# Performance work log

Measured on AMD Instinct MI355X. Metric: run time of the kernel, lower is better.

## Reference

```python
import jax, jax.numpy as jnp
import numpy as np

T, H, I, E, K, L, R = 1024, 1024, 1024, 8, 2, 4, 16
N = 2 * I  # gate_up dim


def setup_inputs() -> dict:
    key = jax.random.key(0)
    ks = jax.random.split(key, 12)
    tw = jax.random.uniform(ks[1], (T, K), dtype=jnp.float32) + 0.1
    tw = tw / tw.sum(axis=-1, keepdims=True)  # routing weights sum to 1
    return {
        "hidden_states": jax.random.normal(ks[0], (T, H), dtype=jnp.float32),
        "topk_weights": tw,
        "w13": jax.random.normal(ks[2], (E, N, H), dtype=jnp.float32) * (1.0 / np.sqrt(H)),
        "w2": jax.random.normal(ks[3], (E, H, I), dtype=jnp.float32) * (1.0 / np.sqrt(I)),
        "gate_up_lora_a": jax.random.normal(ks[4], (L, E, R, H), dtype=jnp.float32) * (1.0 / np.sqrt(H)),
        "gate_up_lora_b": jax.random.normal(ks[5], (L, E, N, R), dtype=jnp.float32) * (1.0 / np.sqrt(R)),
        "down_lora_a": jax.random.normal(ks[6], (L, E, R, I), dtype=jnp.float32) * (1.0 / np.sqrt(I)),
        "down_lora_b": jax.random.normal(ks[7], (L, E, H, R), dtype=jnp.float32) * (1.0 / np.sqrt(R)),
        "scalings": jax.random.uniform(ks[8], (L,), dtype=jnp.float32) + 0.5,
        "topk_ids": jax.random.randint(ks[9], (T, K), 0, E, dtype=jnp.int32),
        "lora_indices": jax.random.randint(ks[10], (T,), 0, L, dtype=jnp.int32),
    }


def reference(hidden_states, topk_weights, w13, w2, gate_up_lora_a,
              gate_up_lora_b, down_lora_a, down_lora_b, scalings,
              topk_ids, lora_indices):
    num_tokens, hidden = hidden_states.shape
    num_experts, gate_up_dim, _ = w13.shape
    top_k = topk_ids.shape[1]
    inter = gate_up_dim // 2
    TKp = num_tokens * top_k

    e_flat = topk_ids.reshape(-1)                      # [TK] expert per dispatched pair
    l_flat = jnp.repeat(lora_indices, top_k)           # [TK] adapter per pair
    w_flat = topk_weights.reshape(-1)                  # [TK] routing weight
    x_rep = jnp.repeat(hidden_states, top_k, axis=0)   # [TK, H]

    # ---- grouped gate_up GEMM (base path): cache1[p] = x[p] @ w13[e(p)]^T ----
    cache1 = jnp.zeros((TKp, gate_up_dim), dtype=hidden_states.dtype)
    for ei in range(num_experts):  # small fixed expert count
        mask = (e_flat == ei)[:, None]
        cache1 = cache1 + jnp.where(mask, x_rep @ w13[ei].T, 0.0)

    # ---- per-expert gate_up LoRA delta, injected BEFORE activation ----
    scal = scalings[l_flat][:, None]                   # [TK, 1]
    Ag = gate_up_lora_a[l_flat, e_flat]                # [TK, R, H]
    Bg = gate_up_lora_b[l_flat, e_flat]                # [TK, N, R]
    tmp = jnp.einsum('prh,ph->pr', Ag, x_rep)
    cache1 = cache1 + jnp.einsum('pnr,pr->pn', Bg, tmp) * scal

    # ---- silu_and_mul on (base + lora) ----
    act = jax.nn.silu(cache1[:, :inter]) * cache1[:, inter:]   # [TK, I]

    # ---- grouped down GEMM (base), routed-weight applied ----
    cache3 = jnp.zeros((TKp, hidden), dtype=hidden_states.dtype)
    for ei in range(num_experts):
        mask = (e_flat == ei)[:, None]
        cache3 = cache3 + jnp.where(mask, act @ w2[ei].T, 0.0)
    cache3 = cache3 * w_flat[:, None]

    # ---- per-expert down LoRA delta (weighted by routing weight) ----
    Ad = down_lora_a[l_flat, e_flat]                   # [TK, R, I]
    Bd = down_lora_b[l_flat, e_flat]                   # [TK, H, R]
    tmpd = jnp.einsum('pri,pi->pr', Ad, act)
    cache3 = cache3 + jnp.einsum('phr,pr->ph', Bd, tmpd) * scal * w_flat[:, None]

    # ---- combine expert outputs (moe_sum over top_k slots) ----
    return cache3.reshape(num_tokens, top_k, hidden).sum(axis=1)
```

## Files before the change

kernel.cpp:

```cpp
#include <hip/hip_runtime.h>
#include <stdint.h>

#define Td 1024
#define Hd 1024
#define Id 1024
#define Ed 8
#define Kd 2
#define Ld 4
#define Rd 16
#define Nd 2048
#define TKd (Td*Kd)

typedef __bf16 bf16x8 __attribute__((ext_vector_type(8)));
typedef float f32x4 __attribute__((ext_vector_type(4)));

__device__ __forceinline__ ushort f2bf(float f) {
    uint32_t u = __builtin_bit_cast(uint32_t, f);
    return (ushort)((u + 0x7fffu + ((u >> 16) & 1u)) >> 16);
}
__device__ __forceinline__ float bf2f(ushort u) {
    uint32_t x = ((uint32_t)u) << 16;
    return __builtin_bit_cast(float, x);
}
__device__ __forceinline__ bf16x8 pack8(float4 a, float4 b) {
    bf16x8 r;
    r[0] = (__bf16)a.x; r[1] = (__bf16)a.y; r[2] = (__bf16)a.z; r[3] = (__bf16)a.w;
    r[4] = (__bf16)b.x; r[5] = (__bf16)b.y; r[6] = (__bf16)b.z; r[7] = (__bf16)b.w;
    return r;
}

#define GLOAD_LDS16(g, l) __builtin_amdgcn_global_load_lds( \
    (const __attribute__((address_space(1))) uint32_t*)(const void*)(g), \
    (__attribute__((address_space(3))) uint32_t*)(void*)(l), 16, 0, 0)

#define XB 512
#define CB 384
#define TB 2048
#define ZB 1024
#define PREP_BLOCKS (XB + CB + TB + ZB + 1)

__global__ __launch_bounds__(256) void k_prep(
    const float* __restrict__ hid, const float* __restrict__ gb,
    const float* __restrict__ db, const float* __restrict__ ga,
    const float* __restrict__ sc, const int* __restrict__ tids,
    const int* __restrict__ lidx,
    ushort* __restrict__ xb, ushort* __restrict__ gbbe, ushort* __restrict__ dbbe,
    ushort* __restrict__ tmp1e, float* __restrict__ out,
    int* __restrict__ sorted, int* __restrict__ offs)
{
    __shared__ float tr[Rd];
    __shared__ int cnt[Ed];
    __shared__ int cur[Ed];
    const int b = blockIdx.x, tid = threadIdx.x;

    if (b < XB) {
        int i = b * 256 + tid;
        size_t off = (size_t)i * 8;
        float4 a = *(const float4*)(hid + off);
        float4 c = *(const float4*)(hid + off + 4);
        uint4 o;
        o.x = (uint)f2bf(a.x) | ((uint)f2bf(a.y) << 16);
        o.y = (uint)f2bf(a.z) | ((uint)f2bf(a.w) << 16);
        o.z = (uint)f2bf(c.x) | ((uint)f2bf(c.y) << 16);
        o.w = (uint)f2bf(c.z) | ((uint)f2bf(c.w) << 16);
        *(uint4*)(xb + off) = o;
    } else if (b < XB + CB) {
        constexpr int GR = Ld * Ed * Nd;
        int i = (b - XB) * 256 + tid;
        const float* src; ushort* dst;
        if (i < GR) {
            int l = i >> 14, e = (i >> 11) & 7, n = i & 2047;
            src = gb + (size_t)i * 16;
            dst = gbbe + ((size_t)(e * Nd + n)) * 64 + l * 16;
        } else {
            int j = i - GR;
            int l = j >> 13, e = (j >> 10) & 7, n = j & 1023;
            src = db + (size_t)j * 16;
            dst = dbbe + ((size_t)(e * Id + n)) * 64 + l * 16;
        }
        float4 a0 = *(const float4*)(src);
        float4 a1 = *(const float4*)(src + 4);
        float4 a2 = *(const float4*)(src + 8);
        float4 a3 = *(const float4*)(src + 12);
        uint4 o;
        o.x = (uint)f2bf(a0.x) | ((uint)f2bf(a0.y) << 16);
        o.y = (uint)f2bf(a0.z) | ((uint)f2bf(a0.w) << 16);
        o.z = (uint)f2bf(a1.x) | ((uint)f2bf(a1.y) << 16);
        o.w = (uint)f2bf(a1.z) | ((uint)f2bf(a1.w) << 16);
        *(uint4*)(dst) = o;
        o.x = (uint)f2bf(a2.x) | ((uint)f2bf(a2.y) << 16);
        o.y = (uint)f2bf(a2.z) | ((uint)f2bf(a2.w) << 16);
        o.z = (uint)f2bf(a3.x) | ((uint)f2bf(a3.y) << 16);
        o.w = (uint)f2bf(a3.z) | ((uint)f2bf(a3.w) << 16);
        *(uint4*)(dst + 8) = o;
    } else if (b < XB + CB + TB) {
        const int p = b - XB - CB;
        const int e = tids[p];
        const int l = lidx[p >> 1];
        const float s = sc[l];
        const int r = tid >> 4, q = tid & 15;
        const float* A = ga + (((size_t)l * Ed + e) * Rd + r) * 1024;
        const float* x = hid + (size_t)(p >> 1) * 1024;
        float sum = 0.f;
        #pragma unroll
        for (int i = 0; i < 16; ++i) {
            int h = q * 4 + 64 * i;
            float4 a = *(const float4*)(A + h);
            float4 v = *(const float4*)(x + h);
            sum += a.x * v.x + a.y * v.y + a.z * v.z + a.w * v.w;
        }
        sum += __shfl_xor(sum, 1); sum += __shfl_xor(sum, 2);
        sum += __shfl_xor(sum, 4); sum += __shfl_xor(sum, 8);
        if (q == 0) tr[r] = sum;
        __syncthreads();
        if (tid < 32) {
            int j0 = tid * 2;
            uint v = 0;
            if ((j0 >> 4) == l)
                v = (uint)f2bf(s * tr[j0 & 15]) | ((uint)f2bf(s * tr[(j0 + 1) & 15]) << 16);
            ((uint*)(tmp1e + (size_t)p * 64))[tid] = v;
        }
    } else if (b < XB + CB + TB + ZB) {
        int i = (b - XB - CB - TB) * 256 + tid;
        ((float4*)out)[i] = make_float4(0.f, 0.f, 0.f, 0.f);
    } else {
        if (tid < Ed) cnt[tid] = 0;
        __syncthreads();
        int el[8];
        #pragma unroll
        for (int i = 0; i < 8; ++i) {
            el[i] = tids[tid + i * 256];
            atomicAdd(&cnt[el[i]], 1);
        }
        __syncthreads();
        if (tid == 0) {
            int s = 0;
            for (int e = 0; e < Ed; ++e) { offs[e] = s; cur[e] = s; s += cnt[e]; }
            offs[Ed] = s;
        }
        __syncthreads();
        #pragma unroll
        for (int i = 0; i < 8; ++i) {
            int pos = atomicAdd(&cur[el[i]], 1);
            sorted[pos] = tid + i * 256;
        }
    }
}

__global__ __launch_bounds__(256) void k_tmp_dn(
    const ushort* __restrict__ act, const float* __restrict__ da,
    const float* __restrict__ sc, const int* __restrict__ tids,
    const int* __restrict__ lidx, ushort* __restrict__ tmpde)
{
    const int p = blockIdx.x;
    const int e = tids[p];
    const int l = lidx[p >> 1];
    const float s = sc[l];
    const int tid = threadIdx.x;
    const int r = tid >> 4, q = tid & 15;
    const float* A = da + (((size_t)l * Ed + e) * Rd + r) * 1024;
    const ushort* x = act + (size_t)p * 1024;
    float sum = 0.f;
    #pragma unroll
    for (int i = 0; i < 8; ++i) {
        int h = q * 8 + 128 * i;
        float4 a0 = *(const float4*)(A + h);
        float4 a1 = *(const float4*)(A + h + 4);
        ushort4 v0 = *(const ushort4*)(x + h);
        ushort4 v1 = *(const ushort4*)(x + h + 4);
        sum += a0.x * bf2f(v0.x) + a0.y * bf2f(v0.y) + a0.z * bf2f(v0.z) + a0.w * bf2f(v0.w)
             + a1.x * bf2f(v1.x) + a1.y * bf2f(v1.y) + a1.z * bf2f(v1.z) + a1.w * bf2f(v1.w);
    }
    sum += __shfl_xor(sum, 1); sum += __shfl_xor(sum, 2);
    sum += __shfl_xor(sum, 4); sum += __shfl_xor(sum, 8);
    __shared__ float tr[Rd];
    if (q == 0) tr[r] = sum;
    __syncthreads();
    if (tid < 32) {
        int j0 = tid * 2;
        uint v = 0;
        if ((j0 >> 4) == l)
            v = (uint)f2bf(s * tr[j0 & 15]) | ((uint)f2bf(s * tr[(j0 + 1) & 15]) << 16);
        ((uint*)(tmpde + (size_t)p * 64))[tid] = v;
    }
}

__global__ __launch_bounds__(256) void k_gemm_gu(
    const ushort* __restrict__ xb, const float* __restrict__ w13,
    const ushort* __restrict__ tmp1e, const ushort* __restrict__ gbbe,
    ushort* __restrict__ act, const int* __restrict__ sorted,
    const int* __restrict__ offs)
{
    __shared__ ushort As[2][128][32];
    __shared__ ushort Bs[2][128][32];
    const int tid = threadIdx.x, lane = tid & 63, wave = tid >> 6;
    const int wr = wave >> 1, wc = wave & 1;
    const int fr = lane & 15, fk = (lane >> 4) * 8;

    int off[Ed + 1];
    #pragma unroll
    for (int e = 0; e <= Ed; ++e) off[e] = offs[e];
    int mt[Ed]; int tot = 0;
    #pragma unroll
    for (int e = 0; e < Ed; ++e) {
        mt[e] = (off[e + 1] - off[e] + 127) / 128;
        tot += mt[e] * 16;
    }

    for (int tau = blockIdx.x; tau < tot; tau += gridDim.x) {
        int t = tau, e = 0;
        while (t >= mt[e] * 16) { t -= mt[e] * 16; ++e; }
        const int m0 = off[e] + (t >> 4) * 128;
        const int mend = off[e + 1];
        const int n0 = (t & 15) * 64;

        const ushort *asrc[2], *aesrc[2], *besrc[2];
        #pragma unroll
        for (int r = 0; r < 2; ++r) {
            int c = r * 256 + tid;
            int row = c >> 2, kc = c & 3;
            int aIdx = m0 + row; if (aIdx > mend - 1) aIdx = mend - 1;
            int p = sorted[aIdx];
            asrc[r]  = xb + (size_t)(p >> 1) * 1024 + kc * 8;
            aesrc[r] = tmp1e + (size_t)p * 64 + kc * 8;
            int grow = (row < 64) ? (n0 + row) : (1024 + n0 + row - 64);
            besrc[r] = gbbe + ((size_t)e * Nd + grow) * 64 + kc * 8;
        }
        const int brow = tid >> 1, bhalf = tid & 1;
        const int bg_row = (brow < 64) ? (n0 + brow) : (1024 + n0 + brow - 64);
        const float* bsrc = w13 + ((size_t)e * Nd + bg_row) * 1024 + bhalf * 16;

        f32x4 ag[4][2] = {}, au[4][2] = {};
        auto step = [&](int buf) {
            bf16x8 af[4], bg[2], bu[2];
            #pragma unroll
            for (int mi = 0; mi < 4; ++mi)
                af[mi] = *(const bf16x8*)(&As[buf][wr * 64 + mi * 16 + fr][fk]);
            #pragma unroll
            for (int ni = 0; ni < 2; ++ni) {
                bg[ni] = *(const bf16x8*)(&Bs[buf][wc * 32 + ni * 16 + fr][fk]);
                bu[ni] = *(const bf16x8*)(&Bs[buf][64 + wc * 32 + ni * 16 + fr][fk]);
            }
            #pragma unroll
            for (int mi = 0; mi < 4; ++mi)
                #pragma unroll
                for (int ni = 0; ni < 2; ++ni) {
                    ag[mi][ni] = __builtin_amdgcn_mfma_f32_16x16x32_bf16(af[mi], bg[ni], ag[mi][ni], 0, 0, 0);
                    au[mi][ni] = __builtin_amdgcn_mfma_f32_16x16x32_bf16(af[mi], bu[ni], au[mi][ni], 0, 0, 0);
                }
        };

        #pragma unroll
        for (int r = 0; r < 2; ++r)
            GLOAD_LDS16(asrc[r], (char*)&As[0][0][0] + (r * 256 + wave * 64) * 16);
        {
            float4 y0 = *(const float4*)(bsrc);
            float4 y1 = *(const float4*)(bsrc + 4);
            float4 y2 = *(const float4*)(bsrc + 8);
            float4 y3 = *(const float4*)(bsrc + 12);
            *(bf16x8*)(&Bs[0][brow][bhalf * 16])     = pack8(y0, y1);
            *(bf16x8*)(&Bs[0][brow][bhalf * 16 + 8]) = pack8(y2, y3);
        }
        __syncthreads();

        int buf = 0;
        for (int k0 = 32; k0 < 1024; k0 += 32) {
            #pragma unroll
            for (int r = 0; r < 2; ++r)
                GLOAD_LDS16(asrc[r] + k0, (char*)&As[buf ^ 1][0][0] + (r * 256 + wave * 64) * 16);
            float4 y0 = *(const float4*)(bsrc + k0);
            float4 y1 = *(const float4*)(bsrc + k0 + 4);
            float4 y2 = *(const float4*)(bsrc + k0 + 8);
            float4 y3 = *(const float4*)(bsrc + k0 + 12);

            step(buf);

            *(bf16x8*)(&Bs[buf ^ 1][brow][bhalf * 16])     = pack8(y0, y1);
            *(bf16x8*)(&Bs[buf ^ 1][brow][bhalf * 16 + 8]) = pack8(y2, y3);
            __syncthreads();
            buf ^= 1;
        }
        step(buf);

        #pragma unroll
        for (int es = 0; es < 2; ++es) {
            #pragma unroll
            for (int r = 0; r < 2; ++r) {
                GLOAD_LDS16(aesrc[r] + es * 32, (char*)&As[es][0][0] + (r * 256 + wave * 64) * 16);
                GLOAD_LDS16(besrc[r] + es * 32, (char*)&Bs[es][0][0] + (r * 256 + wave * 64) * 16);
            }
            __syncthreads();
            step(es);
        }

        const int rb = wr * 64 + (lane >> 4) * 4;
        #pragma unroll
        for (int mi = 0; mi < 4; ++mi) {
            #pragma unroll
            for (int j = 0; j < 4; ++j) {
                int sidx = m0 + rb + mi * 16 + j;
                if (sidx < mend) {
                    int p = sorted[sidx];
                    ushort* ar = act + (size_t)p * 1024 + n0 + wc * 32;
                    #pragma unroll
                    for (int ni = 0; ni < 2; ++ni) {
                        float g = ag[mi][ni][j], u = au[mi][ni][j];
                        float v = g / (1.f + __expf(-g)) * u;
                        ar[ni * 16 + fr] = f2bf(v);
                    }
                }
            }
        }
        __syncthreads();
    }
}

__global__ __launch_bounds__(256) void k_gemm_dn(
    const ushort* __restrict__ act, const float* __restrict__ w2,
    const ushort* __restrict__ tmpde, const ushort* __restrict__ dbbe,
    const float* __restrict__ tw, float* __restrict__ out,
    const int* __restrict__ sorted, const int* __restrict__ offs)
{
    __shared__ ushort As[2][128][32];
    __shared__ ushort Bs[2][64][32];
    const int tid = threadIdx.x, lane = tid & 63, wave = tid >> 6;
    const int wr = wave >> 1, wc = wave & 1;
    const int fr = lane & 15, fk = (lane >> 4) * 8;

    int off[Ed + 1];
    #pragma unroll
    for (int e = 0; e <= Ed; ++e) off[e] = offs[e];
    int mt[Ed]; int tot = 0;
    #pragma unroll
    for (int e = 0; e < Ed; ++e) {
        mt[e] = (off[e + 1] - off[e] + 127) / 128;
        tot += mt[e] * 16;
    }

    for (int tau = blockIdx.x; tau < tot; tau += gridDim.x) {
        int t = tau, e = 0;
        while (t >= mt[e] * 16) { t -= mt[e] * 16; ++e; }
        const int m0 = off[e] + (t >> 4) * 128;
        const int mend = off[e + 1];
        const int n0 = (t & 15) * 64;

        const ushort *asrc[2], *aesrc[2], *besrc;
        #pragma unroll
        for (int r = 0; r < 2; ++r) {
            int c = r * 256 + tid;
            int row = c >> 2, kc = c & 3;
            int aIdx = m0 + row; if (aIdx > mend - 1) aIdx = mend - 1;
            int p = sorted[aIdx];
            asrc[r]  = act + (size_t)p * 1024 + kc * 8;
            aesrc[r] = tmpde + (size_t)p * 64 + kc * 8;
        }
        besrc = dbbe + ((size_t)e * Hd + n0 + (tid >> 2)) * 64 + (tid & 3) * 8;
        const int brow = tid >> 2, bq = tid & 3;
        const float* bsrc = w2 + ((size_t)e * Hd + n0 + brow) * 1024 + bq * 8;

        f32x4 acc[4][2] = {};
        auto step = [&](int buf) {
            bf16x8 af[4], bv[2];
            #pragma unroll
            for (int mi = 0; mi < 4; ++mi)
                af[mi] = *(const bf16x8*)(&As[buf][wr * 64 + mi * 16 + fr][fk]);
            #pragma unroll
            for (int ni = 0; ni < 2; ++ni)
                bv[ni] = *(const bf16x8*)(&Bs[buf][wc * 32 + ni * 16 + fr][fk]);
            #pragma unroll
            for (int mi = 0; mi < 4; ++mi)
                #pragma unroll
                for (int ni = 0; ni < 2; ++ni)
                    acc[mi][ni] = __builtin_amdgcn_mfma_f32_16x16x32_bf16(af[mi], bv[ni], acc[mi][ni], 0, 0, 0);
        };

        #pragma unroll
        for (int r = 0; r < 2; ++r)
            GLOAD_LDS16(asrc[r], (char*)&As[0][0][0] + (r * 256 + wave * 64) * 16);
        {
            float4 y0 = *(const float4*)(bsrc);
            float4 y1 = *(const float4*)(bsrc + 4);
            *(bf16x8*)(&Bs[0][brow][bq * 8]) = pack8(y0, y1);
        }
        __syncthreads();

        int buf = 0;
        for (int k0 = 32; k0 < 1024; k0 += 32) {
            #pragma unroll
            for (int r = 0; r < 2; ++r)
                GLOAD_LDS16(asrc[r] + k0, (char*)&As[buf ^ 1][0][0] + (r * 256 + wave * 64) * 16);
            float4 y0 = *(const float4*)(bsrc + k0);
            float4 y1 = *(const float4*)(bsrc + k0 + 4);

            step(buf);

            *(bf16x8*)(&Bs[buf ^ 1][brow][bq * 8]) = pack8(y0, y1);
            __syncthreads();
            buf ^= 1;
        }
        step(buf);

        #pragma unroll
        for (int es = 0; es < 2; ++es) {
            #pragma unroll
            for (int r = 0; r < 2; ++r)
                GLOAD_LDS16(aesrc[r] + es * 32, (char*)&As[es][0][0] + (r * 256 + wave * 64) * 16);
            GLOAD_LDS16(besrc + es * 32, (char*)&Bs[es][0][0] + (wave * 64) * 16);
            __syncthreads();
            step(es);
        }

        const int rb = wr * 64 + (lane >> 4) * 4;
        #pragma unroll
        for (int mi = 0; mi < 4; ++mi) {
            #pragma unroll
            for (int j = 0; j < 4; ++j) {
                int sidx = m0 + rb + mi * 16 + j;
                if (sidx < mend) {
                    int p = sorted[sidx];
                    float w = tw[p];
                    float* orow = out + (size_t)(p >> 1) * 1024 + n0 + wc * 32;
                    #pragma unroll
                    for (int ni = 0; ni < 2; ++ni)
                        atomicAdd(&orow[ni * 16 + fr], w * acc[mi][ni][j]);
                }
            }
        }
        __syncthreads();
    }
}

extern "C" void kernel_launch(void* const* d_in, const int* in_sizes, int n_in,
                              void* d_out, int out_size, void* d_ws, size_t ws_size,
                              hipStream_t stream) {
    const float* hid  = (const float*)d_in[0];
    const float* tw   = (const float*)d_in[1];
    const float* w13  = (const float*)d_in[2];
    const float* w2   = (const float*)d_in[3];
    const float* ga   = (const float*)d_in[4];
    const float* gb   = (const float*)d_in[5];
    const float* da   = (const float*)d_in[6];
    const float* db   = (const float*)d_in[7];
    const float* sc   = (const float*)d_in[8];
    const int*   tids = (const int*)d_in[9];
    const int*   lidx = (const int*)d_in[10];
    float* out = (float*)d_out;

    char* ws = (char*)d_ws;
    ushort* xb     = (ushort*)(ws);
    ushort* gbbe   = (ushort*)(ws + (2ull << 20));
    ushort* dbbe   = (ushort*)(ws + (4ull << 20));
    ushort* tmp1e  = (ushort*)(ws + (5ull << 20));
    ushort* tmpde  = (ushort*)(ws + (5ull << 20) + (256u << 10));
    ushort* act    = (ushort*)(ws + (6ull << 20));
    int*    sorted = (int*)(ws + (10ull << 20));
    int*    offs   = (int*)(ws + (10ull << 20) + TKd * 4);

    k_prep<<<PREP_BLOCKS, 256, 0, stream>>>(hid, gb, db, ga, sc, tids, lidx,
                                            xb, gbbe, dbbe, tmp1e, out, sorted, offs);
    k_gemm_gu<<<512, 256, 0, stream>>>(xb, w13, tmp1e, gbbe, act, sorted, offs);
    k_tmp_dn<<<TKd, 256, 0, stream>>>(act, da, sc, tids, lidx, tmpde);
    k_gemm_dn<<<512, 256, 0, stream>>>(act, w2, tmpde, dbbe, tw, out, sorted, offs);
}
```

Measured before the change: 100.8 us.

## Stream fp32 operands straight to LDS with swizzle, convert to bf16 at fragment load

Result: slower. 156.4 us (+55.2%).

```diff
diff --git a/kernel.cpp b/kernel.cpp
--- a/kernel.cpp
+++ b/kernel.cpp
@@ -33,68 +33,48 @@
     (const __attribute__((address_space(1))) uint32_t*)(const void*)(g), \
     (__attribute__((address_space(3))) uint32_t*)(void*)(l), 16, 0, 0)
 
-#define XB 512
 #define CB 384
 #define TB 2048
 #define ZB 1024
-#define PREP_BLOCKS (XB + CB + TB + ZB + 1)
+#define PREP_BLOCKS (CB + TB + ZB + 1)
 
 __global__ __launch_bounds__(256) void k_prep(
     const float* __restrict__ hid, const float* __restrict__ gb,
     const float* __restrict__ db, const float* __restrict__ ga,
     const float* __restrict__ sc, const int* __restrict__ tids,
     const int* __restrict__ lidx,
-    ushort* __restrict__ xb, ushort* __restrict__ gbbe, ushort* __restrict__ dbbe,
-    ushort* __restrict__ tmp1e, float* __restrict__ out,
-    int* __restrict__ sorted, int* __restrict__ offs)
+    float* __restrict__ gbbe, float* __restrict__ dbbe, float* __restrict__ tmp1e,
+    float* __restrict__ out, int* __restrict__ sorted, int* __restrict__ offs)
 {
     __shared__ float tr[Rd];
     __shared__ int cnt[Ed];
     __shared__ int cur[Ed];
     const int b = blockIdx.x, tid = threadIdx.x;
 
-    if (b < XB) {
+    if (b < CB) {
+        constexpr int GR = Ld * Ed * Nd;
         int i = b * 256 + tid;
-        size_t off = (size_t)i * 8;
-        float4 a = *(const float4*)(hid + off);
-        float4 c = *(const float4*)(hid + off + 4);
-        uint4 o;
-        o.x = (uint)f2bf(a.x) | ((uint)f2bf(a.y) << 16);
-        o.y = (uint)f2bf(a.z) | ((uint)f2bf(a.w) << 16);
-        o.z = (uint)f2bf(c.x) | ((uint)f2bf(c.y) << 16);
-        o.w = (uint)f2bf(c.z) | ((uint)f2bf(c.w) << 16);
-        *(uint4*)(xb + off) = o;
-    } else if (b < XB + CB) {
-        constexpr int GR = Ld * Ed * Nd;
-        int i = (b - XB) * 256 + tid;
-        const float* src; ushort* dst;
+        const float* src; float* dst;
         if (i < GR) {
             int l = i >> 14, e = (i >> 11) & 7, n = i & 2047;
             src = gb + (size_t)i * 16;
             dst = gbbe + ((size_t)(e * Nd + n)) * 64 + l * 16;
         } else {
             int j = i - GR;
-            int l = j >> 13, e = (j >> 10) & 7, n = j & 1023;
+            int l = j >> 13, e = (j >> 10) & 7, h = j & 1023;
             src = db + (size_t)j * 16;
-            dst = dbbe + ((size_t)(e * Id + n)) * 64 + l * 16;
+            dst = dbbe + ((size_t)(e * Id + h)) * 64 + l * 16;
         }
         float4 a0 = *(const float4*)(src);
         float4 a1 = *(const float4*)(src + 4);
         float4 a2 = *(const float4*)(src + 8);
         float4 a3 = *(const float4*)(src + 12);
-        uint4 o;
-        o.x = (uint)f2bf(a0.x) | ((uint)f2bf(a0.y) << 16);
-        o.y = (uint)f2bf(a0.z) | ((uint)f2bf(a0.w) << 16);
-        o.z = (uint)f2bf(a1.x) | ((uint)f2bf(a1.y) << 16);
-        o.w = (uint)f2bf(a1.z) | ((uint)f2bf(a1.w) << 16);
-        *(uint4*)(dst) = o;
-        o.x = (uint)f2bf(a2.x) | ((uint)f2bf(a2.y) << 16);
-        o.y = (uint)f2bf(a2.z) | ((uint)f2bf(a2.w) << 16);
-        o.z = (uint)f2bf(a3.x) | ((uint)f2bf(a3.y) << 16);
-        o.w = (uint)f2bf(a3.z) | ((uint)f2bf(a3.w) << 16);
-        *(uint4*)(dst + 8) = o;
-    } else if (b < XB + CB + TB) {
-        const int p = b - XB - CB;
+        *(float4*)(dst)      = a0;
+        *(float4*)(dst + 4)  = a1;
+        *(float4*)(dst + 8)  = a2;
+        *(float4*)(dst + 12) = a3;
+    } else if (b < CB + TB) {
+        const int p = b - CB;
         const int e = tids[p];
         const int l = lidx[p >> 1];
         const float s = sc[l];
@@ -113,15 +93,11 @@
         sum += __shfl_xor(sum, 4); sum += __shfl_xor(sum, 8);
         if (q == 0) tr[r] = sum;
         __syncthreads();
-        if (tid < 32) {
-            int j0 = tid * 2;
-            uint v = 0;
-            if ((j0 >> 4) == l)
-                v = (uint)f2bf(s * tr[j0 & 15]) | ((uint)f2bf(s * tr[(j0 + 1) & 15]) << 16);
-            ((uint*)(tmp1e + (size_t)p * 64))[tid] = v;
-        }
-    } else if (b < XB + CB + TB + ZB) {
-        int i = (b - XB - CB - TB) * 256 + tid;
+        if (tid < 64) {
+            tmp1e[(size_t)p * 64 + tid] = ((tid >> 4) == l) ? s * tr[tid & 15] : 0.f;
+        }
+    } else if (b < CB + TB + ZB) {
+        int i = (b - CB - TB) * 256 + tid;
         ((float4*)out)[i] = make_float4(0.f, 0.f, 0.f, 0.f);
     } else {
         if (tid < Ed) cnt[tid] = 0;
@@ -186,111 +162,107 @@
 }
 
 __global__ __launch_bounds__(256) void k_gemm_gu(
-    const ushort* __restrict__ xb, const float* __restrict__ w13,
-    const ushort* __restrict__ tmp1e, const ushort* __restrict__ gbbe,
+    const float* __restrict__ hid, const float* __restrict__ w13,
+    const float* __restrict__ tmp1e, const float* __restrict__ gbbe,
     ushort* __restrict__ act, const int* __restrict__ sorted,
     const int* __restrict__ offs)
 {
-    __shared__ ushort As[2][128][32];
-    __shared__ ushort Bs[2][128][32];
+    __shared__ float Af[2][128 * 32];
+    __shared__ float Bf[2][128 * 32];
     const int tid = threadIdx.x, lane = tid & 63, wave = tid >> 6;
     const int wr = wave >> 1, wc = wave & 1;
-    const int fr = lane & 15, fk = (lane >> 4) * 8;
-
-    int off[Ed + 1];
+    const int fr = lane & 15, q = lane >> 4;
+
+    int off[Ed + 1], mt[Ed], pre[Ed + 1];
     #pragma unroll
     for (int e = 0; e <= Ed; ++e) off[e] = offs[e];
-    int mt[Ed]; int tot = 0;
+    pre[0] = 0;
     #pragma unroll
     for (int e = 0; e < Ed; ++e) {
         mt[e] = (off[e + 1] - off[e] + 127) / 128;
-        tot += mt[e] * 16;
-    }
-
-    for (int tau = blockIdx.x; tau < tot; tau += gridDim.x) {
-        int t = tau, e = 0;
-        while (t >= mt[e] * 16) { t -= mt[e] * 16; ++e; }
-        const int m0 = off[e] + (t >> 4) * 128;
+        pre[e + 1] = pre[e] + mt[e] * 16;
+    }
+    const int tot = pre[Ed];
+
+    for (int bid = blockIdx.x; bid < tot; bid += gridDim.x) {
+        int qq = tot >> 3, rr = tot & 7, x = bid & 7, ii = bid >> 3;
+        int tau = (x < rr) ? x * (qq + 1) + ii : rr * (qq + 1) + (x - rr) * qq + ii;
+        int e = 0;
+        while (tau >= pre[e + 1]) ++e;
+        int local = tau - pre[e];
+        int nt = local / mt[e];
+        int mtile = local - nt * mt[e];
+        const int m0 = off[e] + mtile * 128;
         const int mend = off[e + 1];
-        const int n0 = (t & 15) * 64;
-
-        const ushort *asrc[2], *aesrc[2], *besrc[2];
-        #pragma unroll
-        for (int r = 0; r < 2; ++r) {
-            int c = r * 256 + tid;
-            int row = c >> 2, kc = c & 3;
-            int aIdx = m0 + row; if (aIdx > mend - 1) aIdx = mend - 1;
+        const int n0 = nt * 64;
+
+        const float *as[4], *aes[4], *bs[4], *bes[4];
+        #pragma unroll
+        for (int r = 0; r < 4; ++r) {
+            int s = r * 256 + tid;
+            int srow = s >> 3, si = (s & 7) ^ (srow & 7);
+            int aIdx = m0 + srow; if (aIdx > mend - 1) aIdx = mend - 1;
             int p = sorted[aIdx];
-            asrc[r]  = xb + (size_t)(p >> 1) * 1024 + kc * 8;
-            aesrc[r] = tmp1e + (size_t)p * 64 + kc * 8;
-            int grow = (row < 64) ? (n0 + row) : (1024 + n0 + row - 64);
-            besrc[r] = gbbe + ((size_t)e * Nd + grow) * 64 + kc * 8;
-        }
-        const int brow = tid >> 1, bhalf = tid & 1;
-        const int bg_row = (brow < 64) ? (n0 + brow) : (1024 + n0 + brow - 64);
-        const float* bsrc = w13 + ((size_t)e * Nd + bg_row) * 1024 + bhalf * 16;
+            as[r]  = hid + (size_t)(p >> 1) * 1024 + si * 4;
+            aes[r] = tmp1e + (size_t)p * 64 + si * 4;
+            int grow = (srow < 64) ? (n0 + srow) : (1024 + n0 + srow - 64);
+            bs[r]  = w13 + ((size_t)e * Nd + grow) * 1024 + si * 4;
+            bes[r] = gbbe + ((size_t)(e * Nd + grow)) * 64 + si * 4;
+        }
 
         f32x4 ag[4][2] = {}, au[4][2] = {};
+
+        auto stage = [&](int s, int buf) {
+            if (s < 32) {
+                int k0 = s * 32;
+                #pragma unroll
+                for (int r = 0; r < 4; ++r) {
+                    GLOAD_LDS16(as[r] + k0, (char*)&Af[buf][0] + (r * 256 + wave * 64) * 16);
+                    GLOAD_LDS16(bs[r] + k0, (char*)&Bf[buf][0] + (r * 256 + wave * 64) * 16);
+                }
+            } else {
+                int k0 = (s - 32) * 32;
+                #pragma unroll
+                for (int r = 0; r < 4; ++r) {
+                    GLOAD_LDS16(aes[r] + k0, (char*)&Af[buf][0] + (r * 256 + wave * 64) * 16);
+                    GLOAD_LDS16(bes[r] + k0, (char*)&Bf[buf][0] + (r * 256 + wave * 64) * 16);
+                }
+            }
+        };
         auto step = [&](int buf) {
-            bf16x8 af[4], bg[2], bu[2];
+            bf16x8 afv[4], bg[2], bu[2];
+            #pragma unroll
+            for (int mi = 0; mi < 4; ++mi) {
+                int R = wr * 64 + mi * 16 + fr;
+                const float4* base = (const float4*)&Af[buf][R * 32];
+                afv[mi] = pack8(base[(2 * q) ^ (R & 7)], base[(2 * q + 1) ^ (R & 7)]);
+            }
+            #pragma unroll
+            for (int ni = 0; ni < 2; ++ni) {
+                int Rg = wc * 32 + ni * 16 + fr;
+                const float4* bb = (const float4*)&Bf[buf][Rg * 32];
+                bg[ni] = pack8(bb[(2 * q) ^ (Rg & 7)], bb[(2 * q + 1) ^ (Rg & 7)]);
+                int Ru = Rg + 64;
+                const float4* bu_ = (const float4*)&Bf[buf][Ru * 32];
+                bu[ni] = pack8(bu_[(2 * q) ^ (Ru & 7)], bu_[(2 * q + 1) ^ (Ru & 7)]);
+            }
             #pragma unroll
             for (int mi = 0; mi < 4; ++mi)
-                af[mi] = *(const bf16x8*)(&As[buf][wr * 64 + mi * 16 + fr][fk]);
-            #pragma unroll
-            for (int ni = 0; ni < 2; ++ni) {
-                bg[ni] = *(const bf16x8*)(&Bs[buf][wc * 32 + ni * 16 + fr][fk]);
-                bu[ni] = *(const bf16x8*)(&Bs[buf][64 + wc * 32 + ni * 16 + fr][fk]);
-            }
-            #pragma unroll
-            for (int mi = 0; mi < 4; ++mi)
                 #pragma unroll
                 for (int ni = 0; ni < 2; ++ni) {
-                    ag[mi][ni] = __builtin_amdgcn_mfma_f32_16x16x32_bf16(af[mi], bg[ni], ag[mi][ni], 0, 0, 0);
-                    au[mi][ni] = __builtin_amdgcn_mfma_f32_16x16x32_bf16(af[mi], bu[ni], au[mi][ni], 0, 0, 0);
+                    ag[mi][ni] = __builtin_amdgcn_mfma_f32_16x16x32_bf16(afv[mi], bg[ni], ag[mi][ni], 0, 0, 0);
+                    au[mi][ni] = __builtin_amdgcn_mfma_f32_16x16x32_bf16(afv[mi], bu[ni], au[mi][ni], 0, 0, 0);
                 }
         };
 
-        #pragma unroll
-        for (int r = 0; r < 2; ++r)
-            GLOAD_LDS16(asrc[r], (char*)&As[0][0][0] + (r * 256 + wave * 64) * 16);
-        {
-            float4 y0 = *(const float4*)(bsrc);
-            float4 y1 = *(const float4*)(bsrc + 4);
-            float4 y2 = *(const float4*)(bsrc + 8);
-            float4 y3 = *(const float4*)(bsrc + 12);
-            *(bf16x8*)(&Bs[0][brow][bhalf * 16])     = pack8(y0, y1);
-            *(bf16x8*)(&Bs[0][brow][bhalf * 16 + 8]) = pack8(y2, y3);
-        }
-        __syncthreads();
-
+        stage(0, 0);
+        __syncthreads();
         int buf = 0;
-        for (int k0 = 32; k0 < 1024; k0 += 32) {
-            #pragma unroll
-            for (int r = 0; r < 2; ++r)
-                GLOAD_LDS16(asrc[r] + k0, (char*)&As[buf ^ 1][0][0] + (r * 256 + wave * 64) * 16);
-            float4 y0 = *(const float4*)(bsrc + k0);
-            float4 y1 = *(const float4*)(bsrc + k0 + 4);
-            float4 y2 = *(const float4*)(bsrc + k0 + 8);
-            float4 y3 = *(const float4*)(bsrc + k0 + 12);
-
+        for (int s = 0; s < 34; ++s) {
+            if (s < 33) stage(s + 1, buf ^ 1);
             step(buf);
-
-            *(bf16x8*)(&Bs[buf ^ 1][brow][bhalf * 16])     = pack8(y0, y1);
-            *(bf16x8*)(&Bs[buf ^ 1][brow][bhalf * 16 + 8]) = pack8(y2, y3);
             __syncthreads();
             buf ^= 1;
-        }
-        step(buf);
-
-        #pragma unroll
-        for (int es = 0; es < 2; ++es) {
-            #pragma unroll
-            for (int r = 0; r < 2; ++r) {
-                GLOAD_LDS16(aesrc[r] + es * 32, (char*)&As[es][0][0] + (r * 256 + wave * 64) * 16);
-                GLOAD_LDS16(besrc[r] + es * 32, (char*)&Bs[es][0][0] + (r * 256 + wave * 64) * 16);
-            }
-            __syncthreads();
-            step(es);
         }
 
         const int rb = wr * 64 + (lane >> 4) * 4;
@@ -311,103 +283,110 @@
                 }
             }
         }
-        __syncthreads();
     }
 }
 
 __global__ __launch_bounds__(256) void k_gemm_dn(
     const ushort* __restrict__ act, const float* __restrict__ w2,
-    const ushort* __restrict__ tmpde, const ushort* __restrict__ dbbe,
+    const ushort* __restrict__ tmpde, const float* __restrict__ dbbe,
     const float* __restrict__ tw, float* __restrict__ out,
     const int* __restrict__ sorted, const int* __restrict__ offs)
 {
-    __shared__ ushort As[2][128][32];
-    __shared__ ushort Bs[2][64][32];
+    __shared__ ushort As[2][128 * 32];
+    __shared__ float  Bf[2][64 * 32];
     const int tid = threadIdx.x, lane = tid & 63, wave = tid >> 6;
     const int wr = wave >> 1, wc = wave & 1;
-    const int fr = lane & 15, fk = (lane >> 4) * 8;
-
-    int off[Ed + 1];
+    const int fr = lane & 15, q = lane >> 4;
+
+    int off[Ed + 1], mt[Ed], pre[Ed + 1];
     #pragma unroll
     for (int e = 0; e <= Ed; ++e) off[e] = offs[e];
-    int mt[Ed]; int tot = 0;
+    pre[0] = 0;
     #pragma unroll
     for (int e = 0; e < Ed; ++e) {
         mt[e] = (off[e + 1] - off[e] + 127) / 128;
-        tot += mt[e] * 16;
-    }
-
-    for (int tau = blockIdx.x; tau < tot; tau += gridDim.x) {
-        int t = tau, e = 0;
-        while (t >= mt[e] * 16) { t -= mt[e] * 16; ++e; }
-        const int m0 = off[e] + (t >> 4) * 128;
+        pre[e + 1] = pre[e] + mt[e] * 16;
+    }
+    const int tot = pre[Ed];
+
+    for (int bid = blockIdx.x; bid < tot; bid += gridDim.x) {
+        int qq = tot >> 3, rr = tot & 7, x = bid & 7, ii = bid >> 3;
+        int tau = (x < rr) ? x * (qq + 1) + ii : rr * (qq + 1) + (x - rr) * qq + ii;
+        int e = 0;
+        while (tau >= pre[e + 1]) ++e;
+        int local = tau - pre[e];
+        int nt = local / mt[e];
+        int mtile = local - nt * mt[e];
+        const int m0 = off[e] + mtile * 128;
         const int mend = off[e + 1];
-        const int n0 = (t & 15) * 64;
-
-        const ushort *asrc[2], *aesrc[2], *besrc;
+        const int n0 = nt * 64;
+
+        const ushort *as[2], *aes[2];
         #pragma unroll
         for (int r = 0; r < 2; ++r) {
-            int c = r * 256 + tid;
-            int row = c >> 2, kc = c & 3;
-            int aIdx = m0 + row; if (aIdx > mend - 1) aIdx = mend - 1;
+            int s = r * 256 + tid;
+            int srow = s >> 2, si = s & 3;
+            int aIdx = m0 + srow; if (aIdx > mend - 1) aIdx = mend - 1;
             int p = sorted[aIdx];
-            asrc[r]  = act + (size_t)p * 1024 + kc * 8;
-            aesrc[r] = tmpde + (size_t)p * 64 + kc * 8;
-        }
-        besrc = dbbe + ((size_t)e * Hd + n0 + (tid >> 2)) * 64 + (tid & 3) * 8;
-        const int brow = tid >> 2, bq = tid & 3;
-        const float* bsrc = w2 + ((size_t)e * Hd + n0 + brow) * 1024 + bq * 8;
+            as[r]  = act + (size_t)p * 1024 + si * 8;
+            aes[r] = tmpde + (size_t)p * 64 + si * 8;
+        }
+        const float *bs[2], *bes[2];
+        #pragma unroll
+        for (int r = 0; r < 2; ++r) {
+            int s = r * 256 + tid;
+            int srow = s >> 3, si = (s & 7) ^ (srow & 7);
+            bs[r]  = w2 + ((size_t)e * Hd + n0 + srow) * 1024 + si * 4;
+            bes[r] = dbbe + ((size_t)(e * Hd + n0 + srow)) * 64 + si * 4;
+        }
 
         f32x4 acc[4][2] = {};
+
+        auto stage = [&](int s, int buf) {
+            if (s < 32) {
+                int k0 = s * 32;
+                #pragma unroll
+                for (int r = 0; r < 2; ++r) {
+                    GLOAD_LDS16(as[r] + k0, (char*)&As[buf][0] + (r * 256 + wave * 64) * 16);
+                    GLOAD_LDS16(bs[r] + k0, (char*)&Bf[buf][0] + (r * 256 + wave * 64) * 16);
+                }
+            } else {
+                int k0 = (s - 32) * 32;
+                #pragma unroll
+                for (int r = 0; r < 2; ++r) {
+                    GLOAD_LDS16(aes[r] + k0, (char*)&As[buf][0] + (r * 256 + wave * 64) * 16);
+                    GLOAD_LDS16(bes[r] + k0, (char*)&Bf[buf][0] + (r * 256 + wave * 64) * 16);
+                }
+            }
+        };
         auto step = [&](int buf) {
-            bf16x8 af[4], bv[2];
+            bf16x8 afv[4], bv[2];
+            #pragma unroll
+            for (int mi = 0; mi < 4; ++mi) {
+                int R = wr * 64 + mi * 16 + fr;
+                afv[mi] = *(const bf16x8*)((const char*)&As[buf][0] + R * 64 + q * 16);
+            }
+            #pragma unroll
+            for (int ni = 0; ni < 2; ++ni) {
+                int R = wc * 32 + ni * 16 + fr;
+                const float4* bb = (const float4*)&Bf[buf][R * 32];
+                bv[ni] = pack8(bb[(2 * q) ^ (R & 7)], bb[(2 * q + 1) ^ (R & 7)]);
+            }
             #pragma unroll
             for (int mi = 0; mi < 4; ++mi)
-                af[mi] = *(const bf16x8*)(&As[buf][wr * 64 + mi * 16 + fr][fk]);
-            #pragma unroll
-            for (int ni = 0; ni < 2; ++ni)
-                bv[ni] = *(const bf16x8*)(&Bs[buf][wc * 32 + ni * 16 + fr][fk]);
-            #pragma unroll
-            for (int mi = 0; mi < 4; ++mi)
                 #pragma unroll
                 for (int ni = 0; ni < 2; ++ni)
-                    acc[mi][ni] = __builtin_amdgcn_mfma_f32_16x16x32_bf16(af[mi], bv[ni], acc[mi][ni], 0, 0, 0);
+                    acc[mi][ni] = __builtin_amdgcn_mfma_f32_16x16x32_bf16(afv[mi], bv[ni], acc[mi][ni], 0, 0, 0);
         };
 
-        #pragma unroll
-        for (int r = 0; r < 2; ++r)
-            GLOAD_LDS16(asrc[r], (char*)&As[0][0][0] + (r * 256 + wave * 64) * 16);
-        {
-            float4 y0 = *(const float4*)(bsrc);
-            float4 y1 = *(const float4*)(bsrc + 4);
-            *(bf16x8*)(&Bs[0][brow][bq * 8]) = pack8(y0, y1);
-        }
-        __syncthreads();
-
+        stage(0, 0);
+        __syncthreads();
         int buf = 0;
-        for (int k0 = 32; k0 < 1024; k0 += 32) {
-            #pragma unroll
-            for (int r = 0; r < 2; ++r)
-                GLOAD_LDS16(asrc[r] + k0, (char*)&As[buf ^ 1][0][0] + (r * 256 + wave * 64) * 16);
-            float4 y0 = *(const float4*)(bsrc + k0);
-            float4 y1 = *(const float4*)(bsrc + k0 + 4);
-
+        for (int s = 0; s < 34; ++s) {
+            if (s < 33) stage(s + 1, buf ^ 1);
             step(buf);
-
-            *(bf16x8*)(&Bs[buf ^ 1][brow][bq * 8]) = pack8(y0, y1);
             __syncthreads();
             buf ^= 1;
-        }
-        step(buf);
-
-        #pragma unroll
-        for (int es = 0; es < 2; ++es) {
-            #pragma unroll
-            for (int r = 0; r < 2; ++r)
-                GLOAD_LDS16(aesrc[r] + es * 32, (char*)&As[es][0][0] + (r * 256 + wave * 64) * 16);
-            GLOAD_LDS16(besrc + es * 32, (char*)&Bs[es][0][0] + (wave * 64) * 16);
-            __syncthreads();
-            step(es);
         }
 
         const int rb = wr * 64 + (lane >> 4) * 4;
@@ -426,7 +405,6 @@
                 }
             }
         }
-        __syncthreads();
     }
 }
 
@@ -447,18 +425,17 @@
     float* out = (float*)d_out;
 
     char* ws = (char*)d_ws;
-    ushort* xb     = (ushort*)(ws);
-    ushort* gbbe   = (ushort*)(ws + (2ull << 20));
-    ushort* dbbe   = (ushort*)(ws + (4ull << 20));
-    ushort* tmp1e  = (ushort*)(ws + (5ull << 20));
-    ushort* tmpde  = (ushort*)(ws + (5ull << 20) + (256u << 10));
-    ushort* act    = (ushort*)(ws + (6ull << 20));
-    int*    sorted = (int*)(ws + (10ull << 20));
-    int*    offs   = (int*)(ws + (10ull << 20) + TKd * 4);
+    float*  gbbe   = (float*)(ws);
+    float*  dbbe   = (float*)(ws + (4ull << 20));
+    float*  tmp1e  = (float*)(ws + (6ull << 20));
+    ushort* tmpde  = (ushort*)(ws + (6ull << 20) + (512u << 10));
+    ushort* act    = (ushort*)(ws + (7ull << 20));
+    int*    sorted = (int*)(ws + (11ull << 20));
+    int*    offs   = (int*)(ws + (11ull << 20) + TKd * 4);
 
     k_prep<<<PREP_BLOCKS, 256, 0, stream>>>(hid, gb, db, ga, sc, tids, lidx,
-                                            xb, gbbe, dbbe, tmp1e, out, sorted, offs);
-    k_gemm_gu<<<512, 256, 0, stream>>>(xb, w13, tmp1e, gbbe, act, sorted, offs);
+                                            gbbe, dbbe, tmp1e, out, sorted, offs);
+    k_gemm_gu<<<512, 256, 0, stream>>>(hid, w13, tmp1e, gbbe, act, sorted, offs);
     k_tmp_dn<<<TKd, 256, 0, stream>>>(act, da, sc, tids, lidx, tmpde);
     k_gemm_dn<<<512, 256, 0, stream>>>(act, w2, tmpde, dbbe, tw, out, sorted, offs);
 }
```
